# Kernel optimization log

Hardware: AMD Instinct MI355X
Metric: run time of the kernel (lower is better)

Reference implementation:

```python
import jax, jax.numpy as jnp
import numpy as np

N, C, H = 4096, 768, 12
HD = C // H
SCALE = HD ** -0.5


def setup_inputs() -> dict:
    key = jax.random.key(0)
    k1, k2, k3 = jax.random.split(key, 3)
    x = jax.random.normal(k1, (N, C), dtype=jnp.float32)
    w_qkv = jax.random.normal(k2, (C, 3 * C), dtype=jnp.float32) * (C ** -0.5)
    w_proj = jax.random.normal(k3, (C, C), dtype=jnp.float32) * (C ** -0.5)
    b_proj = jnp.zeros((C,), dtype=jnp.float32)
    return {"x": x, "w_qkv": w_qkv, "w_proj": w_proj, "b_proj": b_proj}


def reference(x, w_qkv, w_proj, b_proj):
    n, c = x.shape
    # fused QKV projection (qkv_bias=False): [N, 3C] -> [3, H, N, hd]
    qkv = (x @ w_qkv).reshape(n, 3, H, HD)
    qkv = jnp.transpose(qkv, (1, 2, 0, 3))  # (3, H, N, hd)
    q, k, v = qkv[0], qkv[1], qkv[2]
    # scaled dot-product attention per head: (H, N, N)
    attn = jnp.einsum('hnd,hmd->hnm', q, k) * SCALE
    attn = jax.nn.softmax(attn, axis=-1)
    # attn_drop is identity (rate=0, eval mode)
    out = jnp.einsum('hnm,hmd->hnd', attn, v)          # (H, N, hd)
    out = jnp.transpose(out, (1, 0, 2)).reshape(n, c)  # (N, C)
    # output projection (bias by default in nn.Dense); proj_drop identity
    return out @ w_proj + b_proj
```

## Files before the change

kernel.cpp:

```cpp
#include <hip/hip_runtime.h>

#define N_TOK 4096
#define C_DIM 768
#define H_NUM 12
#define QKV_N 2304

typedef __attribute__((ext_vector_type(8))) short bf16x8;
typedef __attribute__((ext_vector_type(4))) float f32x4;
typedef __attribute__((ext_vector_type(16))) float f32x16;
typedef __attribute__((ext_vector_type(4))) unsigned int u32x4;

static __device__ __forceinline__ unsigned short f2bf(float f) {
  unsigned u = __builtin_bit_cast(unsigned, f);
  u += 0x7FFF + ((u >> 16) & 1);
  return (unsigned short)(u >> 16);
}

static __device__ __forceinline__ float bf2f(unsigned short u) {
  return __builtin_bit_cast(float, (unsigned)u << 16);
}

static __device__ __forceinline__ float exp2_fast(float x) {
  float r; asm("v_exp_f32 %0, %1" : "=v"(r) : "v"(x)); return r;
}

#define GLOAD_LDS16(g, l)                                                     \
  __builtin_amdgcn_global_load_lds(                                           \
      (const __attribute__((address_space(1))) void*)(g),                     \
      (__attribute__((address_space(3))) void*)(l), 16, 0, 0)

#define Q_SCALE 0.18033688011112042f

__global__ __launch_bounds__(256) void conv_bf16(
    const float* __restrict__ in, unsigned short* __restrict__ out, int n8) {
  const int i = blockIdx.x * 256 + threadIdx.x;
  if (i >= n8) return;
  const float4 a = reinterpret_cast<const float4*>(in)[i * 2];
  const float4 b = reinterpret_cast<const float4*>(in)[i * 2 + 1];
  unsigned short tmp[8] = {f2bf(a.x), f2bf(a.y), f2bf(a.z), f2bf(a.w),
                           f2bf(b.x), f2bf(b.y), f2bf(b.z), f2bf(b.w)};
  reinterpret_cast<bf16x8*>(out)[i] = *reinterpret_cast<bf16x8*>(tmp);
}

__global__ __launch_bounds__(256) void transpose_cvt(
    const float* __restrict__ in, unsigned short* __restrict__ out,
    int K, int N) {
  __shared__ unsigned short T[64][65];
  const int t = threadIdx.x;
  const int k0 = blockIdx.y * 64, n0 = blockIdx.x * 64;
  {
    const int r = t >> 2, qd = t & 3;
#pragma unroll
    for (int i = 0; i < 4; ++i) {
      const int c = qd * 16 + i * 4;
      const float4 v = *reinterpret_cast<const float4*>(
          &in[(size_t)(k0 + r) * N + n0 + c]);
      T[r][c + 0] = f2bf(v.x); T[r][c + 1] = f2bf(v.y);
      T[r][c + 2] = f2bf(v.z); T[r][c + 3] = f2bf(v.w);
    }
  }
  __syncthreads();
#pragma unroll
  for (int i = 0; i < 2; ++i) {
    const int cid = t + i * 256;
    const int rn = cid >> 3, cx = cid & 7;
    unsigned short tmp[8];
#pragma unroll
    for (int j = 0; j < 8; ++j) tmp[j] = T[cx * 8 + j][rn];
    *reinterpret_cast<bf16x8*>(&out[(size_t)(n0 + rn) * K + k0 + cx * 8]) =
        *reinterpret_cast<bf16x8*>(tmp);
  }
}

__global__ __launch_bounds__(256) void gemm_qkv_bf16(
    const unsigned short* __restrict__ A, const unsigned short* __restrict__ Bt,
    unsigned short* __restrict__ qw, unsigned short* __restrict__ kw,
    unsigned short* __restrict__ vw) {
  __shared__ unsigned short As[128 * 32];
  __shared__ unsigned short Bs[128 * 32];
  const int t = threadIdx.x;
  const int lane = t & 63, wid = t >> 6;
  const int lr = lane & 15, lg = lane >> 4;
  const int lid = blockIdx.y * 18 + blockIdx.x;
  const int swz = (lid & 7) * 72 + (lid >> 3);
  const int m_base = (swz / 18) * 128, n_base = (swz % 18) * 128;
  const int wm = (wid >> 1) * 64, wn = (wid & 1) * 64;
  const int c_row = lane >> 2;
  const int c_col = (lane & 3) * 8;

  f32x4 acc[4][4];
#pragma unroll
  for (int mt = 0; mt < 4; ++mt)
#pragma unroll
    for (int nt = 0; nt < 4; ++nt) acc[mt][nt] = (f32x4){0.f, 0.f, 0.f, 0.f};

  for (int kt = 0; kt < 24; ++kt) {
    const int k0 = kt * 32;
    __syncthreads();
#pragma unroll
    for (int i = 0; i < 2; ++i) {
      const int ch = wid * 2 + i;
      GLOAD_LDS16(&A[(size_t)(m_base + ch * 16 + c_row) * 768 + k0 + c_col],
                  &As[ch * 512]);
      GLOAD_LDS16(&Bt[(size_t)(n_base + ch * 16 + c_row) * 768 + k0 + c_col],
                  &Bs[ch * 512]);
    }
    __syncthreads();
    bf16x8 af[4], bfr[4];
#pragma unroll
    for (int mt = 0; mt < 4; ++mt)
      af[mt] = *reinterpret_cast<const bf16x8*>(&As[(wm + mt * 16 + lr) * 32 + lg * 8]);
#pragma unroll
    for (int nt = 0; nt < 4; ++nt)
      bfr[nt] = *reinterpret_cast<const bf16x8*>(&Bs[(wn + nt * 16 + lr) * 32 + lg * 8]);
#pragma unroll
    for (int mt = 0; mt < 4; ++mt)
#pragma unroll
      for (int nt = 0; nt < 4; ++nt)
        acc[mt][nt] = __builtin_amdgcn_mfma_f32_16x16x32_bf16(af[mt], bfr[nt],
                                                              acc[mt][nt], 0, 0, 0);
  }
#pragma unroll
  for (int mt = 0; mt < 4; ++mt)
#pragma unroll
    for (int nt = 0; nt < 4; ++nt)
#pragma unroll
      for (int r = 0; r < 4; ++r) {
        const int m = m_base + wm + mt * 16 + lg * 4 + r;
        const int c = n_base + wn + nt * 16 + lr;
        const float v = acc[mt][nt][r];
        const int which = c / 768;
        const int cc = c - which * 768;
        const int h = cc >> 6, d = cc & 63;
        if (which == 0) {
          qw[((size_t)h * N_TOK + m) * 64 + d] = f2bf(v * Q_SCALE);
        } else if (which == 1) {
          kw[((size_t)h * N_TOK + m) * 64 + d] = f2bf(v);
        } else {
          vw[((size_t)h * 64 + d) * N_TOK + m] = f2bf(v);
        }
      }
}

__global__ __launch_bounds__(256) void gemm_proj_bf16(
    const unsigned short* __restrict__ A, const unsigned short* __restrict__ Bt,
    const float* __restrict__ bias, float* __restrict__ out) {
  __shared__ unsigned short As[128 * 32];
  __shared__ unsigned short Bs[128 * 32];
  const int t = threadIdx.x;
  const int lane = t & 63, wid = t >> 6;
  const int lr = lane & 15, lg = lane >> 4;
  const int lid = blockIdx.y * 6 + blockIdx.x;
  const int swz = (lid & 7) * 24 + (lid >> 3);
  const int m_base = (swz / 6) * 128, n_base = (swz % 6) * 128;
  const int wm = (wid >> 1) * 64, wn = (wid & 1) * 64;
  const int c_row = lane >> 2;
  const int c_col = (lane & 3) * 8;

  f32x4 acc[4][4];
#pragma unroll
  for (int mt = 0; mt < 4; ++mt)
#pragma unroll
    for (int nt = 0; nt < 4; ++nt) acc[mt][nt] = (f32x4){0.f, 0.f, 0.f, 0.f};

  for (int kt = 0; kt < 24; ++kt) {
    const int k0 = kt * 32;
    __syncthreads();
#pragma unroll
    for (int i = 0; i < 2; ++i) {
      const int ch = wid * 2 + i;
      GLOAD_LDS16(&A[(size_t)(m_base + ch * 16 + c_row) * 768 + k0 + c_col],
                  &As[ch * 512]);
      GLOAD_LDS16(&Bt[(size_t)(n_base + ch * 16 + c_row) * 768 + k0 + c_col],
                  &Bs[ch * 512]);
    }
    __syncthreads();
    bf16x8 af[4], bfr[4];
#pragma unroll
    for (int mt = 0; mt < 4; ++mt)
      af[mt] = *reinterpret_cast<const bf16x8*>(&As[(wm + mt * 16 + lr) * 32 + lg * 8]);
#pragma unroll
    for (int nt = 0; nt < 4; ++nt)
      bfr[nt] = *reinterpret_cast<const bf16x8*>(&Bs[(wn + nt * 16 + lr) * 32 + lg * 8]);
#pragma unroll
    for (int mt = 0; mt < 4; ++mt)
#pragma unroll
      for (int nt = 0; nt < 4; ++nt)
        acc[mt][nt] = __builtin_amdgcn_mfma_f32_16x16x32_bf16(af[mt], bfr[nt],
                                                              acc[mt][nt], 0, 0, 0);
  }
#pragma unroll
  for (int nt = 0; nt < 4; ++nt) {
    const int n = n_base + wn + nt * 16 + lr;
    const float bv = bias[n];
#pragma unroll
    for (int mt = 0; mt < 4; ++mt)
#pragma unroll
      for (int r = 0; r < 4; ++r) {
        const int m = m_base + wm + mt * 16 + lg * 4 + r;
        out[(size_t)m * 768 + n] = acc[mt][nt][r] + bv;
      }
  }
}

__global__ __launch_bounds__(256) void attn_kernel(
    const unsigned short* __restrict__ qw, const unsigned short* __restrict__ kw,
    const unsigned short* __restrict__ vw, unsigned short* __restrict__ po0,
    unsigned short* __restrict__ po1, float* __restrict__ lw) {
  __shared__ unsigned short smem[9216];
  const int t = threadIdx.x;
  const int lane = t & 63;
  const int qsub = t >> 6;
  const int q31 = lane & 31;
  const int hi = lane >> 5;
  const int swz = (blockIdx.x & 7) * 96 + (blockIdx.x >> 3);
  const int h = swz >> 6;
  const int rem = swz & 63;
  const int half = rem >> 5;
  const int qst = rem & 31;
  const int q0 = qst * 128 + qsub * 32;

  unsigned short* Ks = smem;
  unsigned short* Vs = smem + 4608;

  const unsigned short* kbase = &kw[(size_t)h * N_TOK * 64];
  const unsigned short* vbase = &vw[(size_t)h * 64 * N_TOK];
  const int kv0 = half * 2048;

  bf16x8 qf[4];
#pragma unroll
  for (int ks = 0; ks < 4; ++ks)
    qf[ks] = *reinterpret_cast<const bf16x8*>(
        &qw[((size_t)h * N_TOK + q0 + q31) * 64 + ks * 16 + hi * 8]);

  f32x16 acc0, acc1;
#pragma unroll
  for (int r = 0; r < 16; ++r) { acc0[r] = 0.f; acc1[r] = 0.f; }
  float l_run = 0.f;

  const int srow0 = t >> 3;
  const int srow1 = (t + 256) >> 3;
  const int sseg = (t & 7) * 8;

  bf16x8 kst[2], vst[2];
  {
    kst[0] = *reinterpret_cast<const bf16x8*>(&kbase[(size_t)(kv0 + srow0) * 64 + sseg]);
    kst[1] = *reinterpret_cast<const bf16x8*>(&kbase[(size_t)(kv0 + srow1) * 64 + sseg]);
    vst[0] = *reinterpret_cast<const bf16x8*>(&vbase[(size_t)srow0 * N_TOK + kv0 + sseg]);
    vst[1] = *reinterpret_cast<const bf16x8*>(&vbase[(size_t)srow1 * N_TOK + kv0 + sseg]);
  }

  for (int kvt = 0; kvt < 32; ++kvt) {
    const int kv = kv0 + kvt * 64;
    __syncthreads();
    *reinterpret_cast<bf16x8*>(&Ks[srow0 * 72 + sseg]) = kst[0];
    *reinterpret_cast<bf16x8*>(&Ks[srow1 * 72 + sseg]) = kst[1];
    *reinterpret_cast<bf16x8*>(&Vs[srow0 * 72 + sseg]) = vst[0];
    *reinterpret_cast<bf16x8*>(&Vs[srow1 * 72 + sseg]) = vst[1];
    __syncthreads();
    const int kvn = (kvt + 1 < 32) ? kv + 64 : kv0;
    kst[0] = *reinterpret_cast<const bf16x8*>(&kbase[(size_t)(kvn + srow0) * 64 + sseg]);
    kst[1] = *reinterpret_cast<const bf16x8*>(&kbase[(size_t)(kvn + srow1) * 64 + sseg]);
    vst[0] = *reinterpret_cast<const bf16x8*>(&vbase[(size_t)srow0 * N_TOK + kvn + sseg]);
    vst[1] = *reinterpret_cast<const bf16x8*>(&vbase[(size_t)srow1 * N_TOK + kvn + sseg]);

#pragma unroll
    for (int ct = 0; ct < 2; ++ct) {
      f32x16 s;
#pragma unroll
      for (int r = 0; r < 16; ++r) s[r] = 0.f;
      __builtin_amdgcn_s_setprio(1);
#pragma unroll
      for (int ks = 0; ks < 4; ++ks) {
        const bf16x8 kf = *reinterpret_cast<const bf16x8*>(
            &Ks[(ct * 32 + q31) * 72 + ks * 16 + hi * 8]);
        s = __builtin_amdgcn_mfma_f32_32x32x16_bf16(kf, qf[ks], s, 0, 0, 0);
      }
      __builtin_amdgcn_s_setprio(0);

      float p[16];
#pragma unroll
      for (int r = 0; r < 16; ++r) p[r] = exp2_fast(s[r]);
      float s8[8];
#pragma unroll
      for (int r = 0; r < 8; ++r) s8[r] = p[r] + p[r + 8];
#pragma unroll
      for (int r = 0; r < 4; ++r) s8[r] = s8[r] + s8[r + 4];
      l_run += (s8[0] + s8[1]) + (s8[2] + s8[3]);

      unsigned dw[8];
#pragma unroll
      for (int m2 = 0; m2 < 8; ++m2)
        asm("v_cvt_pk_bf16_f32 %0, %1, %2"
            : "=v"(dw[m2]) : "v"(p[2 * m2]), "v"(p[2 * m2 + 1]));
      asm("v_permlane32_swap_b32 %0, %1" : "+v"(dw[0]), "+v"(dw[2]));
      asm("v_permlane32_swap_b32 %0, %1" : "+v"(dw[1]), "+v"(dw[3]));
      asm("v_permlane32_swap_b32 %0, %1" : "+v"(dw[4]), "+v"(dw[6]));
      asm("v_permlane32_swap_b32 %0, %1" : "+v"(dw[5]), "+v"(dw[7]));

      __builtin_amdgcn_s_setprio(1);
#pragma unroll
      for (int ksl = 0; ksl < 2; ++ksl) {
        u32x4 u;
        u.x = dw[ksl * 4 + 0]; u.y = dw[ksl * 4 + 1];
        u.z = dw[ksl * 4 + 2]; u.w = dw[ksl * 4 + 3];
        const bf16x8 pa = __builtin_bit_cast(bf16x8, u);
        const int kg = ct * 2 + ksl;
        const bf16x8 vf0 = *reinterpret_cast<const bf16x8*>(
            &Vs[q31 * 72 + kg * 16 + hi * 8]);
        const bf16x8 vf1 = *reinterpret_cast<const bf16x8*>(
            &Vs[(32 + q31) * 72 + kg * 16 + hi * 8]);
        acc0 = __builtin_amdgcn_mfma_f32_32x32x16_bf16(pa, vf0, acc0, 0, 0, 0);
        acc1 = __builtin_amdgcn_mfma_f32_32x32x16_bf16(pa, vf1, acc1, 0, 0, 0);
      }
      __builtin_amdgcn_s_setprio(0);
    }
  }

  l_run += __shfl_xor(l_run, 32);
  const float linv = 1.0f / l_run;
  unsigned short* pout = half ? po1 : po0;
#pragma unroll
  for (int r = 0; r < 16; ++r) {
    const int crow = (r & 3) + 8 * (r >> 2) + 4 * hi;
    const float iv = __shfl(linv, crow);
    const size_t base = (size_t)(q0 + crow) * C_DIM + h * 64;
    pout[base + q31] = f2bf(acc0[r] * iv);
    pout[base + 32 + q31] = f2bf(acc1[r] * iv);
  }
  if (hi == 0) lw[half * 49152 + h * 4096 + q0 + q31] = l_run;
}

__global__ __launch_bounds__(256) void attn_merge(
    unsigned short* __restrict__ po0, const unsigned short* __restrict__ po1,
    const float* __restrict__ lw) {
  const int i = blockIdx.x * 256 + threadIdx.x;
  const int base = i * 8;
  const int q = base / 768;
  const int c = base - q * 768;
  const int h = c >> 6;
  const float l0 = lw[h * 4096 + q];
  const float l1 = lw[49152 + h * 4096 + q];
  const float w = 1.0f / (l0 + l1);
  const float w0 = l0 * w, w1 = l1 * w;
  const bf16x8 a = *reinterpret_cast<const bf16x8*>(&po0[base]);
  const bf16x8 b = *reinterpret_cast<const bf16x8*>(&po1[base]);
  unsigned short tmp[8];
#pragma unroll
  for (int j = 0; j < 8; ++j)
    tmp[j] = f2bf(w0 * bf2f((unsigned short)a[j]) +
                  w1 * bf2f((unsigned short)b[j]));
  *reinterpret_cast<bf16x8*>(&po0[base]) = *reinterpret_cast<bf16x8*>(tmp);
}

extern "C" void kernel_launch(void* const* d_in, const int* in_sizes, int n_in,
                              void* d_out, int out_size, void* d_ws, size_t ws_size,
                              hipStream_t stream) {
  (void)in_sizes; (void)n_in; (void)out_size; (void)ws_size;
  const float* x = (const float*)d_in[0];
  const float* w_qkv = (const float*)d_in[1];
  const float* w_proj = (const float*)d_in[2];
  const float* b_proj = (const float*)d_in[3];
  float* out = (float*)d_out;

  const size_t HNd = (size_t)H_NUM * N_TOK * 64;
  unsigned short* qw = (unsigned short*)d_ws;
  unsigned short* kw = qw + HNd;
  unsigned short* vw = kw + HNd;
  unsigned short* xb = vw + HNd;
  unsigned short* ow = xb;
  unsigned short* wT = xb + HNd;
  unsigned short* wqkvT = wT;
  unsigned short* wprojT = wT;
  unsigned short* po1 = wT + HNd;
  float* lw = (float*)(po1 + HNd);

  conv_bf16<<<dim3((N_TOK * C_DIM / 8 + 255) / 256), 256, 0, stream>>>(
      x, xb, N_TOK * C_DIM / 8);
  transpose_cvt<<<dim3(QKV_N / 64, C_DIM / 64), 256, 0, stream>>>(
      w_qkv, wqkvT, C_DIM, QKV_N);
  gemm_qkv_bf16<<<dim3(QKV_N / 128, N_TOK / 128), 256, 0, stream>>>(
      xb, wqkvT, qw, kw, vw);
  transpose_cvt<<<dim3(C_DIM / 64, C_DIM / 64), 256, 0, stream>>>(
      w_proj, wprojT, C_DIM, C_DIM);
  attn_kernel<<<dim3(768), 256, 0, stream>>>(qw, kw, vw, ow, po1, lw);
  attn_merge<<<dim3(N_TOK * C_DIM / 8 / 256), 256, 0, stream>>>(ow, po1, lw);
  gemm_proj_bf16<<<dim3(C_DIM / 128, N_TOK / 128), 256, 0, stream>>>(
      ow, wprojT, b_proj, out);
}
```

Before: 141.5 us.

## Fuse split-KV merge into proj GEMM and double attention KV tile size

Removes the separate attn_merge kernel and performs the weighted combination of the two KV-half partial outputs while loading the A tile inside the projection GEMM. This drops one launch and a full read-modify-write pass over the attention output. The attention kernel now stages 128 KV rows per iteration instead of 64, halving the number of barrier pairs but doubling LDS use and register staging. The merge is recomputed redundantly across the 6 N-column blocks of the GEMM, and the A tile is loaded synchronously instead of through the direct-to-LDS path.

```diff
diff --git a/kernel.cpp b/kernel.cpp
--- a/kernel.cpp
+++ b/kernel.cpp
@@ -143,7 +143,8 @@
 }
 
 __global__ __launch_bounds__(256) void gemm_proj_bf16(
-    const unsigned short* __restrict__ A, const unsigned short* __restrict__ Bt,
+    const unsigned short* __restrict__ po0, const unsigned short* __restrict__ po1,
+    const float* __restrict__ lw, const unsigned short* __restrict__ Bt,
     const float* __restrict__ bias, float* __restrict__ out) {
   __shared__ unsigned short As[128 * 32];
   __shared__ unsigned short Bs[128 * 32];
@@ -169,10 +170,28 @@
 #pragma unroll
     for (int i = 0; i < 2; ++i) {
       const int ch = wid * 2 + i;
-      GLOAD_LDS16(&A[(size_t)(m_base + ch * 16 + c_row) * 768 + k0 + c_col],
-                  &As[ch * 512]);
       GLOAD_LDS16(&Bt[(size_t)(n_base + ch * 16 + c_row) * 768 + k0 + c_col],
                   &Bs[ch * 512]);
+    }
+#pragma unroll
+    for (int i = 0; i < 2; ++i) {
+      const int ch = wid * 2 + i;
+      const int row = m_base + ch * 16 + c_row;
+      const int col = k0 + c_col;
+      const int hc = col >> 6;
+      const float l0 = lw[hc * 4096 + row];
+      const float l1 = lw[49152 + hc * 4096 + row];
+      const float w = 1.0f / (l0 + l1);
+      const float w0 = l0 * w, w1 = l1 * w;
+      const bf16x8 a = *reinterpret_cast<const bf16x8*>(&po0[(size_t)row * 768 + col]);
+      const bf16x8 b = *reinterpret_cast<const bf16x8*>(&po1[(size_t)row * 768 + col]);
+      unsigned short tmp[8];
+#pragma unroll
+      for (int j = 0; j < 8; ++j)
+        tmp[j] = f2bf(w0 * bf2f((unsigned short)a[j]) +
+                      w1 * bf2f((unsigned short)b[j]));
+      *reinterpret_cast<bf16x8*>(&As[ch * 512 + lane * 8]) =
+          *reinterpret_cast<bf16x8*>(tmp);
     }
     __syncthreads();
     bf16x8 af[4], bfr[4];
@@ -207,7 +226,7 @@
     const unsigned short* __restrict__ qw, const unsigned short* __restrict__ kw,
     const unsigned short* __restrict__ vw, unsigned short* __restrict__ po0,
     unsigned short* __restrict__ po1, float* __restrict__ lw) {
-  __shared__ unsigned short smem[9216];
+  __shared__ unsigned short smem[17920];
   const int t = threadIdx.x;
   const int lane = t & 63;
   const int qsub = t >> 6;
@@ -221,7 +240,7 @@
   const int q0 = qst * 128 + qsub * 32;
 
   unsigned short* Ks = smem;
-  unsigned short* Vs = smem + 4608;
+  unsigned short* Vs = smem + 9216;
 
   const unsigned short* kbase = &kw[(size_t)h * N_TOK * 64];
   const unsigned short* vbase = &vw[(size_t)h * 64 * N_TOK];
@@ -238,34 +257,44 @@
   for (int r = 0; r < 16; ++r) { acc0[r] = 0.f; acc1[r] = 0.f; }
   float l_run = 0.f;
 
-  const int srow0 = t >> 3;
-  const int srow1 = (t + 256) >> 3;
-  const int sseg = (t & 7) * 8;
-
-  bf16x8 kst[2], vst[2];
-  {
-    kst[0] = *reinterpret_cast<const bf16x8*>(&kbase[(size_t)(kv0 + srow0) * 64 + sseg]);
-    kst[1] = *reinterpret_cast<const bf16x8*>(&kbase[(size_t)(kv0 + srow1) * 64 + sseg]);
-    vst[0] = *reinterpret_cast<const bf16x8*>(&vbase[(size_t)srow0 * N_TOK + kv0 + sseg]);
-    vst[1] = *reinterpret_cast<const bf16x8*>(&vbase[(size_t)srow1 * N_TOK + kv0 + sseg]);
-  }
-
-  for (int kvt = 0; kvt < 32; ++kvt) {
-    const int kv = kv0 + kvt * 64;
-    __syncthreads();
-    *reinterpret_cast<bf16x8*>(&Ks[srow0 * 72 + sseg]) = kst[0];
-    *reinterpret_cast<bf16x8*>(&Ks[srow1 * 72 + sseg]) = kst[1];
-    *reinterpret_cast<bf16x8*>(&Vs[srow0 * 72 + sseg]) = vst[0];
-    *reinterpret_cast<bf16x8*>(&Vs[srow1 * 72 + sseg]) = vst[1];
-    __syncthreads();
-    const int kvn = (kvt + 1 < 32) ? kv + 64 : kv0;
-    kst[0] = *reinterpret_cast<const bf16x8*>(&kbase[(size_t)(kvn + srow0) * 64 + sseg]);
-    kst[1] = *reinterpret_cast<const bf16x8*>(&kbase[(size_t)(kvn + srow1) * 64 + sseg]);
-    vst[0] = *reinterpret_cast<const bf16x8*>(&vbase[(size_t)srow0 * N_TOK + kvn + sseg]);
-    vst[1] = *reinterpret_cast<const bf16x8*>(&vbase[(size_t)srow1 * N_TOK + kvn + sseg]);
-
-#pragma unroll
-    for (int ct = 0; ct < 2; ++ct) {
+  const int ksegK = (t & 7) * 8;
+  const int ksegV = (t & 15) * 8;
+
+  bf16x8 kst[4], vst[4];
+#pragma unroll
+  for (int i = 0; i < 4; ++i) {
+    const int krow = (t + i * 256) >> 3;
+    const int vrow = (t + i * 256) >> 4;
+    kst[i] = *reinterpret_cast<const bf16x8*>(
+        &kbase[(size_t)(kv0 + krow) * 64 + ksegK]);
+    vst[i] = *reinterpret_cast<const bf16x8*>(
+        &vbase[(size_t)vrow * N_TOK + kv0 + ksegV]);
+  }
+
+  for (int kvt = 0; kvt < 16; ++kvt) {
+    const int kv = kv0 + kvt * 128;
+    __syncthreads();
+#pragma unroll
+    for (int i = 0; i < 4; ++i) {
+      const int krow = (t + i * 256) >> 3;
+      const int vrow = (t + i * 256) >> 4;
+      *reinterpret_cast<bf16x8*>(&Ks[krow * 72 + ksegK]) = kst[i];
+      *reinterpret_cast<bf16x8*>(&Vs[vrow * 136 + ksegV]) = vst[i];
+    }
+    __syncthreads();
+    const int kvn = (kvt + 1 < 16) ? kv + 128 : kv0;
+#pragma unroll
+    for (int i = 0; i < 4; ++i) {
+      const int krow = (t + i * 256) >> 3;
+      const int vrow = (t + i * 256) >> 4;
+      kst[i] = *reinterpret_cast<const bf16x8*>(
+          &kbase[(size_t)(kvn + krow) * 64 + ksegK]);
+      vst[i] = *reinterpret_cast<const bf16x8*>(
+          &vbase[(size_t)vrow * N_TOK + kvn + ksegV]);
+    }
+
+#pragma unroll
+    for (int ct = 0; ct < 4; ++ct) {
       f32x16 s;
 #pragma unroll
       for (int r = 0; r < 16; ++r) s[r] = 0.f;
@@ -307,9 +336,9 @@
         const bf16x8 pa = __builtin_bit_cast(bf16x8, u);
         const int kg = ct * 2 + ksl;
         const bf16x8 vf0 = *reinterpret_cast<const bf16x8*>(
-            &Vs[q31 * 72 + kg * 16 + hi * 8]);
+            &Vs[q31 * 136 + kg * 16 + hi * 8]);
         const bf16x8 vf1 = *reinterpret_cast<const bf16x8*>(
-            &Vs[(32 + q31) * 72 + kg * 16 + hi * 8]);
+            &Vs[(32 + q31) * 136 + kg * 16 + hi * 8]);
         acc0 = __builtin_amdgcn_mfma_f32_32x32x16_bf16(pa, vf0, acc0, 0, 0, 0);
         acc1 = __builtin_amdgcn_mfma_f32_32x32x16_bf16(pa, vf1, acc1, 0, 0, 0);
       }
@@ -329,28 +358,6 @@
     pout[base + 32 + q31] = f2bf(acc1[r] * iv);
   }
   if (hi == 0) lw[half * 49152 + h * 4096 + q0 + q31] = l_run;
-}
-
-__global__ __launch_bounds__(256) void attn_merge(
-    unsigned short* __restrict__ po0, const unsigned short* __restrict__ po1,
-    const float* __restrict__ lw) {
-  const int i = blockIdx.x * 256 + threadIdx.x;
-  const int base = i * 8;
-  const int q = base / 768;
-  const int c = base - q * 768;
-  const int h = c >> 6;
-  const float l0 = lw[h * 4096 + q];
-  const float l1 = lw[49152 + h * 4096 + q];
-  const float w = 1.0f / (l0 + l1);
-  const float w0 = l0 * w, w1 = l1 * w;
-  const bf16x8 a = *reinterpret_cast<const bf16x8*>(&po0[base]);
-  const bf16x8 b = *reinterpret_cast<const bf16x8*>(&po1[base]);
-  unsigned short tmp[8];
-#pragma unroll
-  for (int j = 0; j < 8; ++j)
-    tmp[j] = f2bf(w0 * bf2f((unsigned short)a[j]) +
-                  w1 * bf2f((unsigned short)b[j]));
-  *reinterpret_cast<bf16x8*>(&po0[base]) = *reinterpret_cast<bf16x8*>(tmp);
 }
 
 extern "C" void kernel_launch(void* const* d_in, const int* in_sizes, int n_in,
@@ -368,7 +375,7 @@
   unsigned short* kw = qw + HNd;
   unsigned short* vw = kw + HNd;
   unsigned short* xb = vw + HNd;
-  unsigned short* ow = xb;
+  unsigned short* po0 = xb;
   unsigned short* wT = xb + HNd;
   unsigned short* wqkvT = wT;
   unsigned short* wprojT = wT;
@@ -383,8 +390,7 @@
       xb, wqkvT, qw, kw, vw);
   transpose_cvt<<<dim3(C_DIM / 64, C_DIM / 64), 256, 0, stream>>>(
       w_proj, wprojT, C_DIM, C_DIM);
-  attn_kernel<<<dim3(768), 256, 0, stream>>>(qw, kw, vw, ow, po1, lw);
-  attn_merge<<<dim3(N_TOK * C_DIM / 8 / 256), 256, 0, stream>>>(ow, po1, lw);
+  attn_kernel<<<dim3(768), 256, 0, stream>>>(qw, kw, vw, po0, po1, lw);
   gemm_proj_bf16<<<dim3(C_DIM / 128, N_TOK / 128), 256, 0, stream>>>(
-      ow, wprojT, b_proj, out);
-}
+      po0, po1, lw, wprojT, b_proj, out);
+}
```

New measurement: 151.3 us. 1.07x slower.
